# Performance work log

Hardware: AMD Instinct MI355X
Metric: run time of the kernel (lower is better)

Reference implementation:

```python
import jax, jax.numpy as jnp
import numpy as np

D_OUT, D_IN = 32768, 1024


def setup_inputs() -> dict:
    key = jax.random.key(0)
    k1, k2, k3, k4, k5 = jax.random.split(key, 5)
    W = jax.random.normal(k1, (D_OUT, D_IN), dtype=jnp.float32)
    Sigma = jax.random.normal(k2, (D_IN, D_IN), dtype=jnp.float32)
    Q = jax.random.normal(k3, (D_OUT, D_IN), dtype=jnp.float32)
    s = jax.random.uniform(k4, (D_OUT, 1), dtype=jnp.float32)
    Theta = jax.random.normal(k5, (D_OUT, D_IN), dtype=jnp.float32)
    return {"W": W, "Sigma": Sigma, "Q": Q, "s": s, "Theta": Theta}


def reference(W, Sigma, Q, s, Theta):
    lamb = 0.05        # last_layer=True
    lamb_reg = 0.0002
    beta = 2.0

    C = W - s * Q                                   # [d_out, d_in], computed in __init__
    # Theta squashing: clip((tanh(Theta)+1)/2 * 1.2 - 0.1, 0, 1)
    Th = jnp.clip((jnp.tanh(Theta) + 1.0) * 0.5 * 1.2 - 0.1, 0.0, 1.0)

    # activation loss: tr(DeltaW Sigma DeltaW^T) = sum((DeltaW @ Sigma) * DeltaW)
    DeltaW = W - s * (Q + Th)
    activation_loss = jnp.sum((DeltaW @ Sigma) * DeltaW)

    # binary regularizer
    binary_reg = lamb_reg * jnp.sum(1.0 - jnp.abs(2.0 * Th - 1.0) ** beta)
    activation_loss = activation_loss + binary_reg

    # geom loss: per-row 1x1 bilinear forms -> K_i = 2 w_i^T Sigma c_i, M_i = 2 w_i^T Sigma th_i
    # ||K_i - s_i M_i||_F^2 = (2*(w_i^T Sigma c_i - s_i * w_i^T Sigma th_i))^2
    WS = W @ Sigma                                  # [d_out, d_in]
    a = jnp.sum(WS * C, axis=1)                     # [d_out]
    b = jnp.sum(WS * Th, axis=1)                    # [d_out]
    geom_loss = jnp.sum((2.0 * (a - s[:, 0] * b)) ** 2)

    total = activation_loss + lamb * geom_loss
    return jnp.reshape(total, (1,))  # torch accumulates geom_loss into a shape-(1,) tensor
```

## Files before the change

### kernel.cpp

```cpp
#include <hip/hip_runtime.h>
#include <cstdint>
#include <cstddef>


#define DOUT 32768
#define DIN  1024
#define PREP_BLOCKS 2048
#define PREP_CHUNKS (DOUT / PREP_BLOCKS)

typedef __bf16 bf16x8 __attribute__((ext_vector_type(8)));
typedef float  f32x4  __attribute__((ext_vector_type(4)));

__device__ __forceinline__ unsigned short f2bf(float f) {
  union { float f; unsigned u; } v; v.f = f;
  unsigned u = v.u + 0x7fffu + ((v.u >> 16) & 1u);
  return (unsigned short)(u >> 16);
}
__device__ __forceinline__ float bf2f(unsigned short b) {
  union { float f; unsigned u; } v; v.u = ((unsigned)b) << 16;
  return v.f;
}

__global__ __launch_bounds__(256) void prep(
    const float4* __restrict__ W4, const float4* __restrict__ Q4,
    const float4* __restrict__ T4, const float* __restrict__ s,
    ushort4* __restrict__ DW4, float* __restrict__ bpart)
{
  const int tid = threadIdx.x;
  const int b   = blockIdx.x;
  float bsum = 0.f;
#pragma unroll 8
  for (int chunk = 0; chunk < PREP_CHUNKS; ++chunk) {
    const int row = b + chunk * PREP_BLOCKS;
    const size_t idx = (size_t)row * 256 + tid;
    const float sv = s[row];
    const float4 wv = W4[idx];
    const float4 qv = Q4[idx];
    const float4 tv = T4[idx];
    ushort4 dp;
#define COMP(fld) { \
    float e  = __builtin_amdgcn_exp2f(tv.fld * 2.885390082f);  \
    float th = 1.1f - 1.2f * __builtin_amdgcn_rcpf(e + 1.f); \
    th = fminf(fmaxf(th, 0.f), 1.f); \
    float um = 2.f * th - 1.f; \
    bsum += 1.f - um * um; \
    dp.fld = f2bf(wv.fld - sv * (qv.fld + th)); }
    COMP(x) COMP(y) COMP(z) COMP(w)
#undef COMP
    DW4[idx] = dp;
  }
  for (int off = 32; off; off >>= 1) bsum += __shfl_down(bsum, off);
  __shared__ float r4[4];
  if ((tid & 63) == 0) r4[tid >> 6] = bsum;
  __syncthreads();
  if (tid == 0) bpart[b] = r4[0] + r4[1] + r4[2] + r4[3];
}

__global__ __launch_bounds__(256) void sconv(const float4* __restrict__ S4,
                                             ushort4* __restrict__ O4)
{
  const int idx = blockIdx.x * 256 + threadIdx.x;
  float4 v = S4[idx];
  ushort4 o;
  o.x = f2bf(v.x); o.y = f2bf(v.y); o.z = f2bf(v.z); o.w = f2bf(v.w);
  O4[idx] = o;
}

__global__ __launch_bounds__(256, 4) void gemm_fused(
    const unsigned short* __restrict__ DW,
    const unsigned short* __restrict__ SG,
    const float* __restrict__ Wf,
    float* __restrict__ t_arr,
    float* __restrict__ acc)
{
  constexpr int K = DIN;
  const int lb  = blockIdx.x;
  const int xcd = lb & 7;
  const int idx = lb >> 3;
  const int m0  = (xcd * 32 + (idx >> 3)) * 128;
  const int n0  = (idx & 7) * 128;
  const int tid = threadIdx.x;
  const int w = tid >> 6;
  const int lane = tid & 63;
  const int wr = w >> 1, wc = w & 1;

  __shared__ unsigned short As[128 * 64];
  __shared__ unsigned short Bs[128 * 64];
  __shared__ float red4[4];

  f32x4 accr[4][4];
#pragma unroll
  for (int i = 0; i < 4; ++i)
#pragma unroll
    for (int j = 0; j < 4; ++j) accr[i][j] = (f32x4){0.f, 0.f, 0.f, 0.f};

  const int l8 = lane >> 3;
  const int lc = ((lane & 7) ^ l8) << 3;

  for (int kt = 0; kt < K / 64; ++kt) {
    const int k0 = kt * 64;
#pragma unroll
    for (int c = 0; c < 4; ++c) {
      const int sub  = c * 4 + w;
      const int rowa = sub * 8 + l8;
      const int ldso = (sub * 64 + lane) * 8;
      const unsigned short* ga = DW + (size_t)(m0 + rowa) * K + (k0 + lc);
      const unsigned short* gb = SG + (size_t)(n0 + rowa) * K + (k0 + lc);
      __builtin_amdgcn_global_load_lds(
          (const __attribute__((address_space(1))) void*)ga,
          (__attribute__((address_space(3))) void*)(As + ldso), 16, 0, 0);
      __builtin_amdgcn_global_load_lds(
          (const __attribute__((address_space(1))) void*)gb,
          (__attribute__((address_space(3))) void*)(Bs + ldso), 16, 0, 0);
    }
    __syncthreads();

    {
      const int q   = lane >> 4;
      const int mr  = lane & 15;
      const int mr7 = mr & 7;
#pragma unroll
      for (int kk = 0; kk < 64; kk += 32) {
        bf16x8 af[4], bfr[4];
        const int cl  = (kk >> 3) + q;
        const int pc8 = ((cl ^ mr7) << 3);
#pragma unroll
        for (int ti = 0; ti < 4; ++ti)
          af[ti] = *(const bf16x8*)&As[(wr * 64 + ti * 16 + mr) * 64 + pc8];
#pragma unroll
        for (int tj = 0; tj < 4; ++tj)
          bfr[tj] = *(const bf16x8*)&Bs[(wc * 64 + tj * 16 + mr) * 64 + pc8];
#pragma unroll
        for (int ti = 0; ti < 4; ++ti)
#pragma unroll
          for (int tj = 0; tj < 4; ++tj)
            accr[ti][tj] = __builtin_amdgcn_mfma_f32_16x16x32_bf16(
                af[ti], bfr[tj], accr[ti][tj], 0, 0, 0);
      }
    }
    __syncthreads();
  }

  const int q  = lane >> 4;
  const int cn = lane & 15;
  float actp = 0.f;
#pragma unroll
  for (int ti = 0; ti < 4; ++ti) {
#pragma unroll
    for (int r = 0; r < 4; ++r) {
      const int i = m0 + wr * 64 + ti * 16 + q * 4 + r;
      const float*          wrow  = Wf + (size_t)i * K;
      const unsigned short* dwrow = DW + (size_t)i * K;
      float ts = 0.f;
#pragma unroll
      for (int tj = 0; tj < 4; ++tj) {
        const int j = n0 + wc * 64 + tj * 16 + cn;
        const float z = accr[ti][tj][r];
        ts   = fmaf(wrow[j], z, ts);
        actp = fmaf(bf2f(dwrow[j]), z, actp);
      }
#pragma unroll
      for (int off = 8; off; off >>= 1) ts += __shfl_xor(ts, off, 16);
      if (cn == 0) atomicAdd(&t_arr[i], ts);
    }
  }
  for (int off = 32; off; off >>= 1) actp += __shfl_down(actp, off);
  if (lane == 0) red4[w] = actp;
  __syncthreads();
  if (tid == 0) atomicAdd(acc, red4[0] + red4[1] + red4[2] + red4[3]);
}

__global__ __launch_bounds__(1024) void finish(const float* __restrict__ t_arr,
                                               const float* __restrict__ bpart,
                                               const float* __restrict__ acc,
                                               float* __restrict__ out)
{
  __shared__ float red[16];
  float g = 0.f;
  for (int i = threadIdx.x; i < DOUT; i += 1024) {
    float t = t_arr[i];
    g = fmaf(0.2f * t, t, g);
  }
  for (int i = threadIdx.x; i < PREP_BLOCKS; i += 1024)
    g = fmaf(2.0e-4f, bpart[i], g);
  for (int off = 32; off; off >>= 1) g += __shfl_down(g, off);
  if ((threadIdx.x & 63) == 0) red[threadIdx.x >> 6] = g;
  __syncthreads();
  if (threadIdx.x == 0) {
    float tot = 0.f;
#pragma unroll
    for (int i = 0; i < 16; ++i) tot += red[i];
    out[0] = acc[0] + tot;
  }
}

extern "C" void kernel_launch(void* const* d_in, const int* in_sizes, int n_in,
                              void* d_out, int out_size, void* d_ws, size_t ws_size,
                              hipStream_t stream) {
  const float* W     = (const float*)d_in[0];
  const float* Sigma = (const float*)d_in[1];
  const float* Q     = (const float*)d_in[2];
  const float* s     = (const float*)d_in[3];
  const float* Theta = (const float*)d_in[4];
  float* out = (float*)d_out;

  char* ws = (char*)d_ws;
  float* acc   = (float*)ws;
  float* t_arr = (float*)(ws + 256);
  float* bpart = (float*)(ws + 256 + 131072);
  unsigned short* SigB = (unsigned short*)(ws + 256 + 131072 + 8192);
  unsigned short* DWb  = (unsigned short*)(ws + 256 + 131072 + 8192 + 2097152);

  hipMemsetAsync(d_ws, 0, 256 + 131072, stream);

  prep<<<PREP_BLOCKS, 256, 0, stream>>>((const float4*)W, (const float4*)Q,
                                        (const float4*)Theta, s, (ushort4*)DWb, bpart);
  sconv<<<(DIN * DIN) / 1024, 256, 0, stream>>>((const float4*)Sigma, (ushort4*)SigB);
  gemm_fused<<<2048, 256, 0, stream>>>(DWb, SigB, W, t_arr, acc);
  finish<<<1, 1024, 0, stream>>>(t_arr, bpart, acc, out);
}
```

Baseline: 502.4 us.

## Fuse DeltaW prep, GEMM and reductions into one persistent-row megakernel

Replaces the separate prep, GEMM and finish kernels with one kernel per 64-row block. Each block computes the bf16 DeltaW rows straight into LDS, streams Sigma through a small double-buffered LDS tile, and reduces the trace and geom terms in-block before atomically adding them to the output. This removes the DeltaW round trip through global memory, the t_arr atomics, two launches and the workspace memset. In exchange the block needs about 128KB of LDS, so only one 512-thread block fits per CU. Per block the GEMM is 64 rows by 1024 columns, which lowers occupancy and adds a barrier at every k-step.

```diff
diff --git a/kernel.cpp b/kernel.cpp
--- a/kernel.cpp
+++ b/kernel.cpp
@@ -5,11 +5,11 @@
 
 #define DOUT 32768
 #define DIN  1024
-#define PREP_BLOCKS 2048
-#define PREP_CHUNKS (DOUT / PREP_BLOCKS)
 
 typedef __bf16 bf16x8 __attribute__((ext_vector_type(8)));
 typedef float  f32x4  __attribute__((ext_vector_type(4)));
+typedef unsigned short u16x8 __attribute__((ext_vector_type(8)));
+typedef unsigned short u16x4 __attribute__((ext_vector_type(4)));
 
 __device__ __forceinline__ unsigned short f2bf(float f) {
   union { float f; unsigned u; } v; v.f = f;
@@ -21,176 +21,167 @@
   return v.f;
 }
 
-__global__ __launch_bounds__(256) void prep(
-    const float4* __restrict__ W4, const float4* __restrict__ Q4,
-    const float4* __restrict__ T4, const float* __restrict__ s,
-    ushort4* __restrict__ DW4, float* __restrict__ bpart)
-{
-  const int tid = threadIdx.x;
-  const int b   = blockIdx.x;
-  float bsum = 0.f;
-#pragma unroll 8
-  for (int chunk = 0; chunk < PREP_CHUNKS; ++chunk) {
-    const int row = b + chunk * PREP_BLOCKS;
-    const size_t idx = (size_t)row * 256 + tid;
-    const float sv = s[row];
-    const float4 wv = W4[idx];
-    const float4 qv = Q4[idx];
-    const float4 tv = T4[idx];
-    ushort4 dp;
-#define COMP(fld) { \
-    float e  = __builtin_amdgcn_exp2f(tv.fld * 2.885390082f);  \
-    float th = 1.1f - 1.2f * __builtin_amdgcn_rcpf(e + 1.f); \
-    th = fminf(fmaxf(th, 0.f), 1.f); \
-    float um = 2.f * th - 1.f; \
-    bsum += 1.f - um * um; \
-    dp.fld = f2bf(wv.fld - sv * (qv.fld + th)); }
-    COMP(x) COMP(y) COMP(z) COMP(w)
-#undef COMP
-    DW4[idx] = dp;
-  }
-  for (int off = 32; off; off >>= 1) bsum += __shfl_down(bsum, off);
-  __shared__ float r4[4];
-  if ((tid & 63) == 0) r4[tid >> 6] = bsum;
-  __syncthreads();
-  if (tid == 0) bpart[b] = r4[0] + r4[1] + r4[2] + r4[3];
-}
-
-__global__ __launch_bounds__(256) void sconv(const float4* __restrict__ S4,
-                                             ushort4* __restrict__ O4)
+__global__ __launch_bounds__(256) void sconv(const f32x4* __restrict__ S4,
+                                             u16x4* __restrict__ O4)
 {
   const int idx = blockIdx.x * 256 + threadIdx.x;
-  float4 v = S4[idx];
-  ushort4 o;
-  o.x = f2bf(v.x); o.y = f2bf(v.y); o.z = f2bf(v.z); o.w = f2bf(v.w);
+  f32x4 v = S4[idx];
+  u16x4 o;
+  o[0] = f2bf(v[0]); o[1] = f2bf(v[1]); o[2] = f2bf(v[2]); o[3] = f2bf(v[3]);
   O4[idx] = o;
 }
 
-__global__ __launch_bounds__(256, 4) void gemm_fused(
-    const unsigned short* __restrict__ DW,
+#define TH(x) ({ float e_ = __builtin_amdgcn_exp2f((x) * 2.885390082f); \
+                 float th_ = 1.1f - 1.2f * __builtin_amdgcn_rcpf(e_ + 1.f); \
+                 fminf(fmaxf(th_, 0.f), 1.f); })
+
+__global__ __launch_bounds__(512, 1) void mega(
+    const float* __restrict__ Wf, const float* __restrict__ Qf,
+    const float* __restrict__ Tf, const float* __restrict__ sv,
     const unsigned short* __restrict__ SG,
-    const float* __restrict__ Wf,
-    float* __restrict__ t_arr,
-    float* __restrict__ acc)
+    float* __restrict__ out)
 {
-  constexpr int K = DIN;
-  const int lb  = blockIdx.x;
-  const int xcd = lb & 7;
-  const int idx = lb >> 3;
-  const int m0  = (xcd * 32 + (idx >> 3)) * 128;
-  const int n0  = (idx & 7) * 128;
-  const int tid = threadIdx.x;
-  const int w = tid >> 6;
+  __shared__ alignas(16) unsigned short As[16 * 4096];
+  __shared__ alignas(16) unsigned char Bs[256 * 80];
+  __shared__ float tred[64][8];
+
+  const int tid  = threadIdx.x;
+  const int m0   = blockIdx.x * 64;
   const int lane = tid & 63;
-  const int wr = w >> 1, wc = w & 1;
-
-  __shared__ unsigned short As[128 * 64];
-  __shared__ unsigned short Bs[128 * 64];
-  __shared__ float red4[4];
-
-  f32x4 accr[4][4];
-#pragma unroll
-  for (int i = 0; i < 4; ++i)
-#pragma unroll
-    for (int j = 0; j < 4; ++j) accr[i][j] = (f32x4){0.f, 0.f, 0.f, 0.f};
-
-  const int l8 = lane >> 3;
-  const int lc = ((lane & 7) ^ l8) << 3;
-
-  for (int kt = 0; kt < K / 64; ++kt) {
-    const int k0 = kt * 64;
-#pragma unroll
-    for (int c = 0; c < 4; ++c) {
-      const int sub  = c * 4 + w;
-      const int rowa = sub * 8 + l8;
-      const int ldso = (sub * 64 + lane) * 8;
-      const unsigned short* ga = DW + (size_t)(m0 + rowa) * K + (k0 + lc);
-      const unsigned short* gb = SG + (size_t)(n0 + rowa) * K + (k0 + lc);
-      __builtin_amdgcn_global_load_lds(
-          (const __attribute__((address_space(1))) void*)ga,
-          (__attribute__((address_space(3))) void*)(As + ldso), 16, 0, 0);
-      __builtin_amdgcn_global_load_lds(
-          (const __attribute__((address_space(1))) void*)gb,
-          (__attribute__((address_space(3))) void*)(Bs + ldso), 16, 0, 0);
-    }
+  const int w    = tid >> 6;
+  const int q    = lane >> 4;
+  const int mr   = lane & 15;
+  const int mr7  = mr & 7;
+
+  float bsum = 0.f;
+  {
+    const int r  = tid >> 3;
+    const int c0 = tid & 7;
+    const float s_r = sv[m0 + r];
+    const size_t rowb = (size_t)(m0 + r) * DIN + c0 * 8;
+    const int abase = r * 64 + ((c0 ^ (r & 7)) << 3);
+#pragma unroll 1
+    for (int j = 0; j < 16; j += 2) {
+      const float* p  = Wf + rowb + (size_t)j * 64;
+      const float* pq = Qf + rowb + (size_t)j * 64;
+      const float* pt = Tf + rowb + (size_t)j * 64;
+      f32x4 wva0 = *(const f32x4*)(p);      f32x4 wva1 = *(const f32x4*)(p + 4);
+      f32x4 wva2 = *(const f32x4*)(p + 64); f32x4 wva3 = *(const f32x4*)(p + 68);
+      f32x4 qva0 = __builtin_nontemporal_load((const f32x4*)(pq));
+      f32x4 qva1 = __builtin_nontemporal_load((const f32x4*)(pq + 4));
+      f32x4 qva2 = __builtin_nontemporal_load((const f32x4*)(pq + 64));
+      f32x4 qva3 = __builtin_nontemporal_load((const f32x4*)(pq + 68));
+      f32x4 tva0 = __builtin_nontemporal_load((const f32x4*)(pt));
+      f32x4 tva1 = __builtin_nontemporal_load((const f32x4*)(pt + 4));
+      f32x4 tva2 = __builtin_nontemporal_load((const f32x4*)(pt + 64));
+      f32x4 tva3 = __builtin_nontemporal_load((const f32x4*)(pt + 68));
+      u16x8 d0, d1;
+#pragma unroll
+      for (int e = 0; e < 4; ++e) {
+        float t0 = TH(tva0[e]); float u0 = 2.f * t0 - 1.f; bsum += 1.f - u0 * u0;
+        d0[e]     = f2bf(wva0[e] - s_r * (qva0[e] + t0));
+        float t1 = TH(tva1[e]); float u1 = 2.f * t1 - 1.f; bsum += 1.f - u1 * u1;
+        d0[e + 4] = f2bf(wva1[e] - s_r * (qva1[e] + t1));
+        float t2 = TH(tva2[e]); float u2 = 2.f * t2 - 1.f; bsum += 1.f - u2 * u2;
+        d1[e]     = f2bf(wva2[e] - s_r * (qva2[e] + t2));
+        float t3 = TH(tva3[e]); float u3 = 2.f * t3 - 1.f; bsum += 1.f - u3 * u3;
+        d1[e + 4] = f2bf(wva3[e] - s_r * (qva3[e] + t3));
+      }
+      *(u16x8*)&As[(j)     * 4096 + abase] = d0;
+      *(u16x8*)&As[(j + 1) * 4096 + abase] = d1;
+    }
+  }
+
+  const int pnrow = tid >> 1;
+  const int pkc   = (tid & 1) * 2;
+  u16x8 pr0, pr1;
+#define PF(np_, kst_) { \
+    const unsigned short* gp_ = SG + (size_t)((np_) * 256 + pnrow) * DIN + (kst_) * 32 + pkc * 8; \
+    pr0 = *(const u16x8*)gp_; pr1 = *(const u16x8*)(gp_ + 8); }
+
+  f32x4 acc[4][2];
+#pragma unroll
+  for (int ti = 0; ti < 4; ++ti) { acc[ti][0] = (f32x4){0,0,0,0}; acc[ti][1] = (f32x4){0,0,0,0}; }
+  float ts[4][4];
+#pragma unroll
+  for (int ti = 0; ti < 4; ++ti)
+#pragma unroll
+    for (int rr = 0; rr < 4; ++rr) ts[ti][rr] = 0.f;
+  float actp = 0.f;
+
+  PF(0, 0);
+#pragma unroll 1
+  for (int st = 0; st < 128; ++st) {
+    const int np  = st >> 5;
+    const int kst = st & 31;
     __syncthreads();
-
+    *(u16x8*)&Bs[pnrow * 80 + pkc * 16]      = pr0;
+    *(u16x8*)&Bs[pnrow * 80 + pkc * 16 + 16] = pr1;
+    if (st < 127) { const int s1 = st + 1; PF(s1 >> 5, s1 & 31); }
+    __syncthreads();
     {
-      const int q   = lane >> 4;
-      const int mr  = lane & 15;
-      const int mr7 = mr & 7;
-#pragma unroll
-      for (int kk = 0; kk < 64; kk += 32) {
-        bf16x8 af[4], bfr[4];
-        const int cl  = (kk >> 3) + q;
-        const int pc8 = ((cl ^ mr7) << 3);
-#pragma unroll
-        for (int ti = 0; ti < 4; ++ti)
-          af[ti] = *(const bf16x8*)&As[(wr * 64 + ti * 16 + mr) * 64 + pc8];
-#pragma unroll
-        for (int tj = 0; tj < 4; ++tj)
-          bfr[tj] = *(const bf16x8*)&Bs[(wc * 64 + tj * 16 + mr) * 64 + pc8];
-#pragma unroll
-        for (int ti = 0; ti < 4; ++ti)
-#pragma unroll
-          for (int tj = 0; tj < 4; ++tj)
-            accr[ti][tj] = __builtin_amdgcn_mfma_f32_16x16x32_bf16(
-                af[ti], bfr[tj], accr[ti][tj], 0, 0, 0);
+      const int CG   = kst * 4 + q;
+      const int aoff = (CG >> 3) * 4096 + (((CG & 7) ^ mr7) << 3) + mr * 64;
+      bf16x8 a0 = *(const bf16x8*)&As[aoff];
+      bf16x8 a1 = *(const bf16x8*)&As[aoff + 16 * 64];
+      bf16x8 a2 = *(const bf16x8*)&As[aoff + 32 * 64];
+      bf16x8 a3 = *(const bf16x8*)&As[aoff + 48 * 64];
+      const int boff = (w * 32 + mr) * 80 + q * 16;
+      bf16x8 b0 = *(const bf16x8*)&Bs[boff];
+      bf16x8 b1 = *(const bf16x8*)&Bs[boff + 16 * 80];
+      acc[0][0] = __builtin_amdgcn_mfma_f32_16x16x32_bf16(a0, b0, acc[0][0], 0, 0, 0);
+      acc[0][1] = __builtin_amdgcn_mfma_f32_16x16x32_bf16(a0, b1, acc[0][1], 0, 0, 0);
+      acc[1][0] = __builtin_amdgcn_mfma_f32_16x16x32_bf16(a1, b0, acc[1][0], 0, 0, 0);
+      acc[1][1] = __builtin_amdgcn_mfma_f32_16x16x32_bf16(a1, b1, acc[1][1], 0, 0, 0);
+      acc[2][0] = __builtin_amdgcn_mfma_f32_16x16x32_bf16(a2, b0, acc[2][0], 0, 0, 0);
+      acc[2][1] = __builtin_amdgcn_mfma_f32_16x16x32_bf16(a2, b1, acc[2][1], 0, 0, 0);
+      acc[3][0] = __builtin_amdgcn_mfma_f32_16x16x32_bf16(a3, b0, acc[3][0], 0, 0, 0);
+      acc[3][1] = __builtin_amdgcn_mfma_f32_16x16x32_bf16(a3, b1, acc[3][1], 0, 0, 0);
+    }
+    if (kst == 31) {
+#pragma unroll
+      for (int ti = 0; ti < 4; ++ti) {
+#pragma unroll
+        for (int rr = 0; rr < 4; ++rr) {
+          const int il  = ti * 16 + q * 4 + rr;
+          const int il7 = (q * 4 + rr) & 7;
+          const float* wrow = Wf + (size_t)(m0 + il) * DIN;
+#pragma unroll
+          for (int tj = 0; tj < 2; ++tj) {
+            const int jj = np * 256 + w * 32 + tj * 16 + mr;
+            const float z = acc[ti][tj][rr];
+            ts[ti][rr] = fmaf(wrow[jj], z, ts[ti][rr]);
+            const int del = (jj >> 6) * 4096 + il * 64 + ((((jj >> 3) & 7) ^ il7) << 3) + (jj & 7);
+            actp = fmaf(bf2f(As[del]), z, actp);
+          }
+        }
       }
-    }
-    __syncthreads();
+#pragma unroll
+      for (int ti = 0; ti < 4; ++ti) { acc[ti][0] = (f32x4){0,0,0,0}; acc[ti][1] = (f32x4){0,0,0,0}; }
+    }
   }
 
-  const int q  = lane >> 4;
-  const int cn = lane & 15;
-  float actp = 0.f;
-#pragma unroll
-  for (int ti = 0; ti < 4; ++ti) {
-#pragma unroll
-    for (int r = 0; r < 4; ++r) {
-      const int i = m0 + wr * 64 + ti * 16 + q * 4 + r;
-      const float*          wrow  = Wf + (size_t)i * K;
-      const unsigned short* dwrow = DW + (size_t)i * K;
-      float ts = 0.f;
-#pragma unroll
-      for (int tj = 0; tj < 4; ++tj) {
-        const int j = n0 + wc * 64 + tj * 16 + cn;
-        const float z = accr[ti][tj][r];
-        ts   = fmaf(wrow[j], z, ts);
-        actp = fmaf(bf2f(dwrow[j]), z, actp);
-      }
-#pragma unroll
-      for (int off = 8; off; off >>= 1) ts += __shfl_xor(ts, off, 16);
-      if (cn == 0) atomicAdd(&t_arr[i], ts);
-    }
-  }
-  for (int off = 32; off; off >>= 1) actp += __shfl_down(actp, off);
-  if (lane == 0) red4[w] = actp;
+  float cpart = actp + 2.0e-4f * bsum;
+  for (int off = 32; off; off >>= 1) cpart += __shfl_down(cpart, off);
+  if (lane == 0) atomicAdd(out, cpart);
+
+#pragma unroll
+  for (int ti = 0; ti < 4; ++ti)
+#pragma unroll
+    for (int rr = 0; rr < 4; ++rr) {
+      float v = ts[ti][rr];
+      v += __shfl_xor(v, 8, 16); v += __shfl_xor(v, 4, 16);
+      v += __shfl_xor(v, 2, 16); v += __shfl_xor(v, 1, 16);
+      if (mr == 0) tred[ti * 16 + q * 4 + rr][w] = v;
+    }
   __syncthreads();
-  if (tid == 0) atomicAdd(acc, red4[0] + red4[1] + red4[2] + red4[3]);
-}
-
-__global__ __launch_bounds__(1024) void finish(const float* __restrict__ t_arr,
-                                               const float* __restrict__ bpart,
-                                               const float* __restrict__ acc,
-                                               float* __restrict__ out)
-{
-  __shared__ float red[16];
-  float g = 0.f;
-  for (int i = threadIdx.x; i < DOUT; i += 1024) {
-    float t = t_arr[i];
-    g = fmaf(0.2f * t, t, g);
-  }
-  for (int i = threadIdx.x; i < PREP_BLOCKS; i += 1024)
-    g = fmaf(2.0e-4f, bpart[i], g);
-  for (int off = 32; off; off >>= 1) g += __shfl_down(g, off);
-  if ((threadIdx.x & 63) == 0) red[threadIdx.x >> 6] = g;
-  __syncthreads();
-  if (threadIdx.x == 0) {
-    float tot = 0.f;
-#pragma unroll
-    for (int i = 0; i < 16; ++i) tot += red[i];
-    out[0] = acc[0] + tot;
+  if (tid < 64) {
+    float t = 0.f;
+#pragma unroll
+    for (int k = 0; k < 8; ++k) t += tred[tid][k];
+    float g = 0.2f * t * t;
+    for (int off = 32; off; off >>= 1) g += __shfl_down(g, off);
+    if (tid == 0) atomicAdd(out, g);
   }
 }
 
@@ -204,18 +195,10 @@
   const float* Theta = (const float*)d_in[4];
   float* out = (float*)d_out;
 
-  char* ws = (char*)d_ws;
-  float* acc   = (float*)ws;
-  float* t_arr = (float*)(ws + 256);
-  float* bpart = (float*)(ws + 256 + 131072);
-  unsigned short* SigB = (unsigned short*)(ws + 256 + 131072 + 8192);
-  unsigned short* DWb  = (unsigned short*)(ws + 256 + 131072 + 8192 + 2097152);
-
-  hipMemsetAsync(d_ws, 0, 256 + 131072, stream);
-
-  prep<<<PREP_BLOCKS, 256, 0, stream>>>((const float4*)W, (const float4*)Q,
-                                        (const float4*)Theta, s, (ushort4*)DWb, bpart);
-  sconv<<<(DIN * DIN) / 1024, 256, 0, stream>>>((const float4*)Sigma, (ushort4*)SigB);
-  gemm_fused<<<2048, 256, 0, stream>>>(DWb, SigB, W, t_arr, acc);
-  finish<<<1, 1024, 0, stream>>>(t_arr, bpart, acc, out);
-}
+  unsigned short* SigB = (unsigned short*)d_ws;
+
+  (void)hipMemsetAsync(d_out, 0, 4, stream);
+
+  sconv<<<(DIN * DIN) / 1024, 256, 0, stream>>>((const f32x4*)Sigma, (u16x4*)SigB);
+  mega<<<DOUT / 64, 512, 0, stream>>>(W, Q, Theta, s, SigB, out);
+}
```

After: 506.0 us. Within noise of the previous version (+0.7%).
